# Kernel optimization log

Hardware: AMD Instinct MI355X
Metric: run time of the kernel (lower is better)

Reference implementation:

```python
import jax, jax.numpy as jnp
import numpy as np

EPS = 1e-08

def _compute_W(V, C, eps=EPS):
    # W = H_k ... H_1, applied sequentially as in the torch loop
    W = jnp.eye(C, dtype=V.dtype)
    def step(W, v):
        v = v / (jnp.linalg.norm(v) + eps)
        # H @ W = W - 2 v (v^T W)
        W = W - 2.0 * jnp.outer(v, v @ W)
        return W, None
    W, _ = jax.lax.scan(step, W, V)
    return W

def setup_inputs() -> dict:
    key = jax.random.key(0)
    k1, k2 = jax.random.split(key)
    x = jax.random.normal(k1, (16, 512, 64, 64), dtype=jnp.float32)
    V = jax.random.normal(k2, (32, 512), dtype=jnp.float32)
    return {"x": x, "V": V}

def reference(x, V):
    B, C, H, Wd = x.shape
    W = _compute_W(V, C)  # [C, C] orthogonal
    # 1x1 conv: out[b,o,h,w] = sum_c W[o,c] * x[b,c,h,w]
    return jnp.einsum('oc,bchw->bohw', W, x)
```

## Files before the change

### kernel.cpp

```cpp
#include <hip/hip_runtime.h>
#include <hip/hip_bf16.h>
#include <stdint.h>
#include <stddef.h>

#define HH_EPS 1e-8f

typedef __attribute__((ext_vector_type(8))) short short8;
typedef __attribute__((ext_vector_type(4))) float f32x4;

#define CDIM 512
#define SDIM 4096
#define BN 64
#define BK 32
#define NSTEP 16
#define BROW 40

__device__ __forceinline__ size_t wt_idx(int o, int c) {
    return ((size_t)((c >> 5) * 32 + (o >> 4)) * 64
            + (size_t)((o & 15) * 4 + ((c >> 3) & 3))) * 8 + (c & 7);
}

__global__ void compute_w(const float* __restrict__ V,
                          __hip_bfloat16* __restrict__ Wt) {
    const int wave = threadIdx.x >> 6;
    const int lane = threadIdx.x & 63;
    const int jA = (blockIdx.x * 4 + wave) * 2;
    const int jB = jA + 1;
    const int ib = lane * 8;

    float wA[8], wB[8];
    #pragma unroll
    for (int r = 0; r < 8; r++) {
        wA[r] = (ib + r == jA) ? 1.0f : 0.0f;
        wB[r] = (ib + r == jB) ? 1.0f : 0.0f;
    }

    float4 c0 = *(const float4*)(V + ib);
    float4 c1 = *(const float4*)(V + ib + 4);

    for (int k = 0; k < 32; k++) {
        const float v[8] = {c0.x, c0.y, c0.z, c0.w, c1.x, c1.y, c1.z, c1.w};
        if (k < 31) {
            c0 = *(const float4*)(V + (size_t)(k + 1) * 512 + ib);
            c1 = *(const float4*)(V + (size_t)(k + 1) * 512 + ib + 4);
        }
        float dA = 0.0f, dB = 0.0f, ss = 0.0f;
        #pragma unroll
        for (int r = 0; r < 8; r++) {
            dA += v[r] * wA[r];
            dB += v[r] * wB[r];
            ss += v[r] * v[r];
        }
        #pragma unroll
        for (int off = 32; off > 0; off >>= 1) {
            dA += __shfl_xor(dA, off);
            dB += __shfl_xor(dB, off);
            ss += __shfl_xor(ss, off);
        }
        const float t = sqrtf(ss) + HH_EPS;
        const float scale = 2.0f / (t * t);
        const float tA = scale * dA, tB = scale * dB;
        #pragma unroll
        for (int r = 0; r < 8; r++) {
            wA[r] -= tA * v[r];
            wB[r] -= tB * v[r];
        }
    }
    #pragma unroll
    for (int r = 0; r < 8; r++) {
        Wt[wt_idx(ib + r, jA)] = __float2bfloat16(wA[r]);
        Wt[wt_idx(ib + r, jB)] = __float2bfloat16(wB[r]);
    }
}

__device__ __forceinline__ void lds_barrier() {
    asm volatile("" ::: "memory");
    __builtin_amdgcn_s_waitcnt(0xC07F);
    __builtin_amdgcn_s_barrier();
    asm volatile("" ::: "memory");
}

__global__ __launch_bounds__(256, 2) void hh_gemm(
    const float* __restrict__ x,
    const short8* __restrict__ Wt16,
    float* __restrict__ out)
{
    __shared__ __attribute__((aligned(16))) __hip_bfloat16 Blds[2][BN * BROW];

    const int tid  = threadIdx.x;
    const int wave = tid >> 6, lane = tid & 63;
    const int quad = lane >> 4, l16 = lane & 15;

    const int bid = blockIdx.x;
    const int b   = bid >> 6;
    const int nt  = bid & 63;
    const int n0  = nt * BN;

    const float* xb = x + (size_t)b * CDIM * SDIM;

    const int bn = tid & 63, kg = tid >> 6;
    const float* xp0 = xb + (size_t)(kg * 8) * SDIM + n0 + bn;

    f32x4 acc[8][4];
    #pragma unroll
    for (int mi = 0; mi < 8; mi++)
        #pragma unroll
        for (int ni = 0; ni < 4; ni++) {
            f32x4 z = {0.0f, 0.0f, 0.0f, 0.0f};
            acc[mi][ni] = z;
        }

    short8 af[2][8];
    float  pfB[2][8];

    auto loadB = [&](int kt, float* dst) {
        const float* p = xp0 + (size_t)kt * BK * SDIM;
        #pragma unroll
        for (int j = 0; j < 8; j++) dst[j] = p[(size_t)j * SDIM];
    };
    auto writeB = [&](int buf, const float* src) {
        short8 pk;
        #pragma unroll
        for (int j = 0; j < 8; j++) {
            __hip_bfloat16 h = __float2bfloat16(src[j]);
            pk[j] = *(short*)&h;
        }
        *(short8*)(&Blds[buf][bn * BROW + kg * 8]) = pk;
    };
    auto loadA = [&](int kt, short8* dst) {
        const short8* p = Wt16 + (size_t)kt * 2048 + (size_t)(wave * 8) * 64
                        + l16 * 4 + quad;
        #pragma unroll
        for (int mi = 0; mi < 8; mi++) dst[mi] = p[mi * 64];
    };

    loadB(0, pfB[0]);
    loadB(1, pfB[1]);
    loadA(0, af[0]);
    writeB(0, pfB[0]);
    lds_barrier();

    auto step = [&](int kt, int p, bool pfb, bool pfa, bool last) {
        if (pfb) loadB(kt + 2, pfB[p]);
        if (pfa) loadA(kt + 1, af[p ^ 1]);
        short8 bfr[4];
        #pragma unroll
        for (int ni = 0; ni < 4; ni++)
            bfr[ni] = *(const short8*)(&Blds[p][(ni * 16 + l16) * BROW + quad * 8]);
        #pragma unroll
        for (int mi = 0; mi < 8; mi++)
            #pragma unroll
            for (int ni = 0; ni < 4; ni++)
                acc[mi][ni] = __builtin_amdgcn_mfma_f32_16x16x32_bf16(
                    af[p][mi], bfr[ni], acc[mi][ni], 0, 0, 0);
        if (!last) {
            writeB(p ^ 1, pfB[p ^ 1]);
            lds_barrier();
        }
    };

    for (int kt = 0; kt < NSTEP - 2; kt += 2) {
        step(kt,     0, true, true, false);
        step(kt + 1, 1, true, true, false);
    }
    step(NSTEP - 2, 0, false, true,  false);
    step(NSTEP - 1, 1, false, false, true);

    float* ob = out + (size_t)b * CDIM * SDIM + n0;
    #pragma unroll
    for (int mi = 0; mi < 8; mi++) {
        #pragma unroll
        for (int ni = 0; ni < 4; ni++) {
            const int col = ni * 16 + l16;
            #pragma unroll
            for (int r = 0; r < 4; r++) {
                const int row = wave * 128 + mi * 16 + quad * 4 + r;
                ob[(size_t)row * SDIM + col] = acc[mi][ni][r];
            }
        }
    }
}

extern "C" void kernel_launch(void* const* d_in, const int* in_sizes, int n_in,
                              void* d_out, int out_size, void* d_ws, size_t ws_size,
                              hipStream_t stream) {
    const float* x = (const float*)d_in[0];
    const float* V = (const float*)d_in[1];
    float* out = (float*)d_out;

    __hip_bfloat16* Wt = (__hip_bfloat16*)d_ws;

    compute_w<<<64, 256, 0, stream>>>(V, Wt);
    hh_gemm<<<1024, 256, 0, stream>>>(x, (const short8*)Wt, out);
}
```

Baseline: 284.0 us.

## Stage W tiles through LDS with async global-to-LDS loads and deepen x prefetch

```diff
diff --git a/kernel.cpp b/kernel.cpp
--- a/kernel.cpp
+++ b/kernel.cpp
@@ -34,7 +34,6 @@
         wA[r] = (ib + r == jA) ? 1.0f : 0.0f;
         wB[r] = (ib + r == jB) ? 1.0f : 0.0f;
     }
-
     float4 c0 = *(const float4*)(V + ib);
     float4 c1 = *(const float4*)(V + ib + 4);
 
@@ -73,19 +72,36 @@
     }
 }
 
+__device__ __forceinline__ void gld_lds16(const void* g, void* l) {
+    __builtin_amdgcn_global_load_lds(
+        (const __attribute__((address_space(1))) uint32_t*)g,
+        (__attribute__((address_space(3))) uint32_t*)l, 16, 0, 0);
+}
+
+template<int N> __device__ __forceinline__ void wait_vm() {
+    __builtin_amdgcn_s_waitcnt((N & 15) | ((N >> 4) << 14) | (7 << 4) | (15 << 8));
+}
+
 __device__ __forceinline__ void lds_barrier() {
-    asm volatile("" ::: "memory");
     __builtin_amdgcn_s_waitcnt(0xC07F);
     __builtin_amdgcn_s_barrier();
-    asm volatile("" ::: "memory");
+}
+
+constexpr int vm_after_A(int kt) {
+    int n = 0;
+    if (kt + 1 < NSTEP) n += 8;
+    if (kt + 2 < NSTEP) n += 8;
+    if (kt + 3 < NSTEP) n += 8;
+    return n;
 }
 
 __global__ __launch_bounds__(256, 2) void hh_gemm(
     const float* __restrict__ x,
-    const short8* __restrict__ Wt16,
+    const __hip_bfloat16* __restrict__ Wt,
     float* __restrict__ out)
 {
-    __shared__ __attribute__((aligned(16))) __hip_bfloat16 Blds[2][BN * BROW];
+    __shared__ __attribute__((aligned(16))) __hip_bfloat16 Albuf[2][512 * BK];
+    __shared__ __attribute__((aligned(16))) __hip_bfloat16 Bbuf[2][BN * BROW];
 
     const int tid  = threadIdx.x;
     const int wave = tid >> 6, lane = tid & 63;
@@ -97,9 +113,8 @@
     const int n0  = nt * BN;
 
     const float* xb = x + (size_t)b * CDIM * SDIM;
-
-    const int bn = tid & 63, kg = tid >> 6;
-    const float* xp0 = xb + (size_t)(kg * 8) * SDIM + n0 + bn;
+    const int bn = tid & 63;
+    const float* xp0 = xb + (size_t)(wave * 8) * SDIM + n0 + bn;
 
     f32x4 acc[8][4];
     #pragma unroll
@@ -110,9 +125,16 @@
             acc[mi][ni] = z;
         }
 
-    short8 af[2][8];
-    float  pfB[2][8];
-
+    float pfB[3][8];
+
+    auto loadA = [&](int kt, int p) {
+        const char* gbase = (const char*)Wt
+            + ((size_t)kt * 32 + (size_t)wave * 8) * 1024 + (size_t)lane * 16;
+        char* lbase = (char*)&Albuf[p][(size_t)(wave * 8) * 512];
+        #pragma unroll
+        for (int i = 0; i < 8; i++)
+            gld_lds16(gbase + (size_t)i * 1024, lbase + (size_t)i * 1024);
+    };
     auto loadB = [&](int kt, float* dst) {
         const float* p = xp0 + (size_t)kt * BK * SDIM;
         #pragma unroll
@@ -125,46 +147,48 @@
             __hip_bfloat16 h = __float2bfloat16(src[j]);
             pk[j] = *(short*)&h;
         }
-        *(short8*)(&Blds[buf][bn * BROW + kg * 8]) = pk;
+        *(short8*)(&Bbuf[buf][bn * BROW + wave * 8]) = pk;
     };
-    auto loadA = [&](int kt, short8* dst) {
-        const short8* p = Wt16 + (size_t)kt * 2048 + (size_t)(wave * 8) * 64
-                        + l16 * 4 + quad;
-        #pragma unroll
-        for (int mi = 0; mi < 8; mi++) dst[mi] = p[mi * 64];
-    };
-
+
+    loadA(0, 0);
     loadB(0, pfB[0]);
     loadB(1, pfB[1]);
-    loadA(0, af[0]);
+    loadB(2, pfB[2]);
     writeB(0, pfB[0]);
     lds_barrier();
 
-    auto step = [&](int kt, int p, bool pfb, bool pfa, bool last) {
-        if (pfb) loadB(kt + 2, pfB[p]);
-        if (pfa) loadA(kt + 1, af[p ^ 1]);
-        short8 bfr[4];
-        #pragma unroll
-        for (int ni = 0; ni < 4; ni++)
-            bfr[ni] = *(const short8*)(&Blds[p][(ni * 16 + l16) * BROW + quad * 8]);
-        #pragma unroll
-        for (int mi = 0; mi < 8; mi++)
-            #pragma unroll
-            for (int ni = 0; ni < 4; ni++)
-                acc[mi][ni] = __builtin_amdgcn_mfma_f32_16x16x32_bf16(
-                    af[p][mi], bfr[ni], acc[mi][ni], 0, 0, 0);
-        if (!last) {
-            writeB(p ^ 1, pfB[p ^ 1]);
-            lds_barrier();
-        }
-    };
-
-    for (int kt = 0; kt < NSTEP - 2; kt += 2) {
-        step(kt,     0, true, true, false);
-        step(kt + 1, 1, true, true, false);
-    }
-    step(NSTEP - 2, 0, false, true,  false);
-    step(NSTEP - 1, 1, false, false, true);
+#define DO_STEP(KT)                                                            \
+    {                                                                          \
+        constexpr int p = (KT) & 1;                                            \
+        if constexpr ((KT) + 1 < NSTEP) loadA((KT) + 1, p ^ 1);                \
+        if constexpr ((KT) + 3 < NSTEP) loadB((KT) + 3, pfB[(KT) % 3]);        \
+        wait_vm<vm_after_A(KT)>();    \
+        short8 afr[8], bfr[4];                                                 \
+        _Pragma("unroll")                                                      \
+        for (int mi = 0; mi < 8; mi++)                                         \
+            afr[mi] = *(const short8*)(&Albuf[p][(wave * 8 + mi) * 512         \
+                                                 + (l16 * 4 + quad) * 8]);     \
+        _Pragma("unroll")                                                      \
+        for (int ni = 0; ni < 4; ni++)                                         \
+            bfr[ni] = *(const short8*)(&Bbuf[p][(ni * 16 + l16) * BROW         \
+                                                + quad * 8]);                  \
+        _Pragma("unroll")                                                      \
+        for (int mi = 0; mi < 8; mi++)                                         \
+            _Pragma("unroll")                                                  \
+            for (int ni = 0; ni < 4; ni++)                                     \
+                acc[mi][ni] = __builtin_amdgcn_mfma_f32_16x16x32_bf16(         \
+                    afr[mi], bfr[ni], acc[mi][ni], 0, 0, 0);                   \
+        if constexpr ((KT) + 1 < NSTEP) {                                      \
+            writeB(p ^ 1, pfB[((KT) + 1) % 3]);                                \
+            lds_barrier();                                                     \
+        }                                                                      \
+    }
+
+    DO_STEP(0)  DO_STEP(1)  DO_STEP(2)  DO_STEP(3)
+    DO_STEP(4)  DO_STEP(5)  DO_STEP(6)  DO_STEP(7)
+    DO_STEP(8)  DO_STEP(9)  DO_STEP(10) DO_STEP(11)
+    DO_STEP(12) DO_STEP(13) DO_STEP(14) DO_STEP(15)
+#undef DO_STEP
 
     float* ob = out + (size_t)b * CDIM * SDIM + n0;
     #pragma unroll
@@ -191,5 +215,5 @@
     __hip_bfloat16* Wt = (__hip_bfloat16*)d_ws;
 
     compute_w<<<64, 256, 0, stream>>>(V, Wt);
-    hh_gemm<<<1024, 256, 0, stream>>>(x, (const short8*)Wt, out);
-}
+    hh_gemm<<<1024, 256, 0, stream>>>(x, Wt, out);
+}
```

Result: faster. 273.7 us (-3.7%).
